# Performance work log

Measured on AMD Instinct MI355X. Metric: run time of the kernel, lower is better.

Reference implementation:

```python
import jax, jax.numpy as jnp
import numpy as np

B, CIN, H, W = 32, 1, 512, 512
PATCH = 16
PW, PH = H // PATCH, W // PATCH  # 32, 32
S = PW * PH                      # 1024 tokens
C = 256
L = 8
POOL = 4
OUT_IDX = (2, 4, 6)
EPS = 1e-5


def setup_inputs() -> dict:
    key = jax.random.key(0)
    ks = jax.random.split(key, 10)
    sc = 1.0 / np.sqrt(C).astype(np.float32)
    return {
        "image": jax.random.normal(ks[0], (B, CIN, H, W), jnp.float32),
        "conv_w": jax.random.normal(ks[1], (C, CIN), jnp.float32),
        "conv_b": jnp.zeros((C,), jnp.float32),
        "feat_w": jax.random.normal(ks[2], (C, C), jnp.float32) * sc,
        "feat_b": jnp.zeros((C,), jnp.float32),
        "ln_s": jnp.ones((L, C), jnp.float32),
        "ln_b": jnp.zeros((L, C), jnp.float32),
        "wq": jax.random.normal(ks[3], (L, C, C), jnp.float32) * sc,
        "bq": jnp.zeros((L, C), jnp.float32),
        "wk": jax.random.normal(ks[4], (L, C, C), jnp.float32) * sc,
        "bk": jnp.zeros((L, C), jnp.float32),
        "wv": jax.random.normal(ks[5], (L, C, C), jnp.float32) * sc,
        "bv": jnp.zeros((L, C), jnp.float32),
        "wf": jax.random.normal(ks[6], (L, C, C), jnp.float32) * sc,
        "bf": jnp.zeros((L, C), jnp.float32),
        "wa": jax.random.normal(ks[7], (L, C, 2 * C), jnp.float32) * sc,
        "ba": jnp.zeros((L, 2 * C), jnp.float32),
    }


def _to_spatial(t):  # [B,S,C] -> [B,C,PW,PH]
    return t.transpose(0, 2, 1).reshape(t.shape[0], C, PW, PH)


def _to_seq(t):  # [B,C,PW,PH] -> [B,S,C]
    return t.reshape(t.shape[0], C, S).transpose(0, 2, 1)


def _layernorm(x, s, b):
    mu = x.mean(-1, keepdims=True)
    var = x.var(-1, keepdims=True)
    return (x - mu) * jax.lax.rsqrt(var + EPS) * s + b


def _attention(x, Wq, bq, Wk, bk, Wv, bv):
    d = np.float32(1.0 / np.sqrt(C))
    Q = _to_spatial(jax.nn.sigmoid(x @ Wq + bq))
    K = _to_spatial(jax.nn.sigmoid(x @ Wk + bk))
    V = _to_spatial(jax.nn.sigmoid(x @ Wv + bv))
    # avg_pool2d with kernel (POOL, 1): pool rows of the patch grid
    qp = Q.reshape(B, C, PW // POOL, POOL, PH).mean(3)
    kp = K.reshape(B, C, PW // POOL, POOL, PH).mean(3)
    # dual softmax low-rank factorization, per channel
    Qk = jax.nn.softmax(d * jnp.einsum('ncik,ncjk->ncij', Q, kp), axis=-1)   # [B,C,PW,PW/POOL]
    Kq = jax.nn.softmax(d * jnp.einsum('ncik,ncjk->ncij', qp, K), axis=-1)   # [B,C,PW/POOL,PW]
    Kqv = jnp.einsum('ncik,nckj->ncij', Kq, V)                               # [B,C,PW/POOL,PH]
    return _to_seq(jnp.einsum('ncik,nckj->ncij', Qk, Kqv))                   # [B,S,C]


def _forward(image, conv_w, conv_b, feat_w, feat_b, ln_s, ln_b,
             wq, bq, wk, bk, wv, bv, wf, bf, wa, ba):
    # Conv2d(kernel=1, stride=patch) == strided subsample + 1x1 projection
    xs = image[:, :, ::PATCH, ::PATCH]                                       # [B,1,PW,PH]
    emb = jnp.einsum('bihw,oi->bohw', xs, conv_w) + conv_b[None, :, None, None]
    x = jnp.tanh(_to_seq(emb) @ feat_w + feat_b)                             # [B,S,C]
    hid, att = [], []
    for l in range(L):
        tn = _layernorm(x, ln_s[l], ln_b[l])
        a = _attention(tn, wq[l], bq[l], wk[l], bk[l], wv[l], bv[l])
        ta = x + a
        # FiLM adaptive norm: sigmoid linear -> interleaved (scale, shift) pairs
        sh = jax.nn.sigmoid(ta @ wa[l] + ba[l]).reshape(B, S, C, 2)
        tn2 = sh[..., 0] * ta + sh[..., 1]
        x = jax.nn.relu(tn2 @ wf[l] + bf[l]) + ta
        if l in OUT_IDX:
            hid.append(x)
            att.append(ta)
    # pack: [last; 3 intermediate hiddens; 3 attention residuals] -> [7,B,S,C]
    return jnp.concatenate([x[None], jnp.stack(hid), jnp.stack(att)], axis=0)


def reference(image, conv_w, conv_b, feat_w, feat_b, ln_s, ln_b,
              wq, bq, wk, bk, wv, bv, wf, bf, wa, ba):
    return _forward(image, conv_w, conv_b, feat_w, feat_b, ln_s, ln_b,
                    wq, bq, wk, bk, wv, bv, wf, bf, wa, ba)
```

## Files before the change

kernel.cpp:

```cpp
#include <hip/hip_runtime.h>
#include <hip/hip_bf16.h>
#include <cstdint>
#include <cstddef>

#define B_ 32
#define C_ 256
#define S_ 1024
#define L_ 8

typedef unsigned short bf16_t;
typedef __attribute__((ext_vector_type(8))) short s8v;
typedef __attribute__((ext_vector_type(4))) short s4v;
typedef __attribute__((ext_vector_type(4))) float f4v;

static __device__ __forceinline__ float b2f(bf16_t v) {
    unsigned int u = ((unsigned int)v) << 16;
    float f;
    __builtin_memcpy(&f, &u, 4);
    return f;
}
static __device__ __forceinline__ bf16_t f2b(float f) {
    unsigned int u;
    __builtin_memcpy(&u, &f, 4);
    u += 0x7fffu + ((u >> 16) & 1u);
    return (bf16_t)(u >> 16);
}
static __device__ __forceinline__ float sigmoidf_(float x) {
    return 1.0f / (1.0f + __expf(-x));
}
static __device__ __forceinline__ void gload_lds16(const void* g, void* l) {
    __builtin_amdgcn_global_load_lds((const __attribute__((address_space(1))) void*)g,
                                     (__attribute__((address_space(3))) void*)l, 16, 0, 0);
}


__global__ void fuse_wb_k(const float* __restrict__ cw, const float* __restrict__ cb,
                          const float* __restrict__ fwm, const float* __restrict__ fbv,
                          float* __restrict__ fw, float* __restrict__ fb) {
    int c = threadIdx.x;
    float a = 0.f, bs = 0.f;
    for (int o = 0; o < C_; o++) {
        float f = fwm[o * C_ + c];
        a += cw[o] * f;
        bs += cb[o] * f;
    }
    fw[c] = a;
    fb[c] = bs + fbv[c];
}

__global__ __launch_bounds__(256) void wtrans_k(const float* __restrict__ wq, const float* __restrict__ wk,
                                                const float* __restrict__ wv, const float* __restrict__ wf,
                                                const float* __restrict__ wa, const float* __restrict__ ln_s,
                                                bf16_t* __restrict__ WT) {
    __shared__ float t[32][33];
    int z = blockIdx.z, l = z / 6, tp = z - l * 6;
    const float* src;
    int ld, cmul, coff;
    if (tp < 4) {
        const float* bases[4] = {wq, wk, wv, wf};
        src = bases[tp] + (size_t)l * 65536;
        ld = 256; cmul = 1; coff = 0;
    } else {
        src = wa + (size_t)l * 131072;
        ld = 512; cmul = 2; coff = tp - 4;
    }
    const float* g = ln_s + l * 256;
    bf16_t* dst = WT + ((size_t)l * 6 + tp) * 65536;
    int k0 = blockIdx.y * 32, m0 = blockIdx.x * 32;
    int tx = threadIdx.x & 31, ty = threadIdx.x >> 5;
#pragma unroll
    for (int r = 0; r < 4; ++r) {
        int k = k0 + ty + 8 * r;
        float v = src[(size_t)k * ld + (m0 + tx) * cmul + coff];
        if (tp < 3) v *= g[k];
        t[ty + 8 * r][tx] = v;
    }
    __syncthreads();
#pragma unroll
    for (int r = 0; r < 4; ++r)
        dst[(size_t)(m0 + ty + 8 * r) * 256 + k0 + tx] = f2b(t[tx][ty + 8 * r]);
}

__global__ __launch_bounds__(256) void colsum_k(const bf16_t* __restrict__ WT,
                                                const float* __restrict__ wq, const float* __restrict__ wk,
                                                const float* __restrict__ wv,
                                                const float* __restrict__ bq, const float* __restrict__ bk,
                                                const float* __restrict__ bv,
                                                const float* __restrict__ ln_b,
                                                float* __restrict__ csum, float* __restrict__ bias2) {
    int m = threadIdx.x, mat = blockIdx.x, l = blockIdx.y;
    const bf16_t* wt = WT + ((size_t)l * 6 + mat) * 65536 + (size_t)m * 256;
    float cs = 0.f;
    for (int k = 0; k < 256; k += 8) {
        s8v u = *(const s8v*)(wt + k);
#pragma unroll
        for (int j = 0; j < 8; ++j) cs += b2f((bf16_t)u[j]);
    }
    const float* worig = (mat == 0 ? wq : mat == 1 ? wk : wv) + (size_t)l * 65536;
    const float* borig = (mat == 0 ? bq : mat == 1 ? bk : bv) + l * 256;
    const float* lb = ln_b + l * 256;
    float bb = 0.f;
    for (int k = 0; k < 256; ++k) bb += lb[k] * worig[(size_t)k * 256 + m];
    int o = (l * 3 + mat) * 256 + m;
    csum[o] = cs;
    bias2[o] = bb + borig[m];
}

__global__ __launch_bounds__(256) void embed_k(const float* __restrict__ img, const float* __restrict__ fw,
                                               const float* __restrict__ fb, bf16_t* __restrict__ X,
                                               float* __restrict__ SUM0, float* __restrict__ SUM1) {
    int wid = threadIdx.x >> 6, lane = threadIdx.x & 63;
    int row = blockIdx.x * 4 + wid;
    int b = row >> 10, s = row & 1023;
    float xv = img[(size_t)b * 262144 + (size_t)(s >> 5) * 8192 + (s & 31) * 16];
    f4v fwv = *(const f4v*)(fw + lane * 4);
    f4v fbv = *(const f4v*)(fb + lane * 4);
    s4v o;
    float sum = 0.f, sq = 0.f;
#pragma unroll
    for (int j = 0; j < 4; ++j) {
        float v = tanhf(xv * fwv[j] + fbv[j]);
        float vb = b2f(f2b(v));
        o[j] = (short)f2b(v);
        sum += vb;
        sq += vb * vb;
    }
    *(s4v*)(X + (size_t)row * 256 + lane * 4) = o;
#pragma unroll
    for (int off = 32; off > 0; off >>= 1) {
        sum += __shfl_xor(sum, off);
        sq += __shfl_xor(sq, off);
    }
    if (lane == 0) {
        SUM0[2 * row] = sum;
        SUM0[2 * row + 1] = sq;
        SUM1[2 * row] = 0.f;
        SUM1[2 * row + 1] = 0.f;
    }
}

template <int MODE, bool HID>
__global__ __launch_bounds__(256) void mm_k(const bf16_t* Ain,
                                            const bf16_t* __restrict__ W0,
                                            const bf16_t* __restrict__ W1,
                                            const float* __restrict__ bias0,
                                            const float* __restrict__ csP,
                                            const float* __restrict__ sumIn,
                                            const bf16_t* ta,
                                            bf16_t* O0, bf16_t* O1, bf16_t* O2,
                                            float* __restrict__ hid,
                                            float* __restrict__ sumOut,
                                            float* __restrict__ sumZero) {
    constexpr int LDSZ = (MODE == 0) ? 34816 : 32768;
    __shared__ char lds[LDSZ];
    char* XS = lds;
    char* WS0 = lds + 16384;
    char* WS1 = lds + 24576;
    const int tid = threadIdx.x, lane = tid & 63, wid = tid >> 6;
    const int wrow = wid >> 1, wcol = wid & 1;
    const int s0 = blockIdx.y * 128, mt0 = blockIdx.x * 64, b = blockIdx.z;

    if constexpr (MODE == 2) {
        int bid = ((blockIdx.z * gridDim.y) + blockIdx.y) * gridDim.x + blockIdx.x;
        if (tid < 64) sumZero[bid * 64 + tid] = 0.f;
    }

    const int lr8 = lane >> 3;
    const int cb0 = ((lane & 7) << 4) ^ (lr8 << 4);

    const char* Ag = (const char*)Ain + (((size_t)b * 1024 + s0) * 256) * 2 + cb0;
    const char* Wg0 = (const char*)W0 + ((size_t)mt0 * 256) * 2 + cb0;
    const char* Wg1 = (const char*)W1 + ((size_t)mt0 * 256) * 2 + cb0;

    f4v acc[4][2] = {};
    f4v acc1[4][2] = {};

    for (int kt = 0; kt < 4; ++kt) {
        const char* ga = Ag + kt * 128;
#pragma unroll
        for (int q = 0; q < 4; ++q) {
            int r0 = wid * 32 + q * 8;
            gload_lds16(ga + (size_t)(r0 + lr8) * 512, XS + r0 * 128);
        }
        const char* gw = Wg0 + kt * 128;
#pragma unroll
        for (int p = 0; p < 2; ++p) {
            int r0 = wid * 16 + p * 8;
            gload_lds16(gw + (size_t)(r0 + lr8) * 512, WS0 + r0 * 128);
        }
        if constexpr (MODE == 1) {
            const char* gw1 = Wg1 + kt * 128;
#pragma unroll
            for (int p = 0; p < 2; ++p) {
                int r0 = wid * 16 + p * 8;
                gload_lds16(gw1 + (size_t)(r0 + lr8) * 512, WS1 + r0 * 128);
            }
        }
        __syncthreads();
#pragma unroll
        for (int kk = 0; kk < 2; ++kk) {
            const int cb = kk * 64 + ((lane >> 4) << 4);
            s8v av[4];
#pragma unroll
            for (int mi = 0; mi < 4; ++mi) {
                int r = wrow * 64 + mi * 16 + (lane & 15);
                av[mi] = *(const s8v*)(XS + r * 128 + (cb ^ ((r & 7) << 4)));
            }
            s8v bv[2], bw[2];
#pragma unroll
            for (int ni = 0; ni < 2; ++ni) {
                int m = wcol * 32 + ni * 16 + (lane & 15);
                bv[ni] = *(const s8v*)(WS0 + m * 128 + (cb ^ ((m & 7) << 4)));
                if constexpr (MODE == 1)
                    bw[ni] = *(const s8v*)(WS1 + m * 128 + (cb ^ ((m & 7) << 4)));
            }
#pragma unroll
            for (int mi = 0; mi < 4; ++mi)
#pragma unroll
                for (int ni = 0; ni < 2; ++ni) {
                    acc[mi][ni] = __builtin_amdgcn_mfma_f32_16x16x32_bf16(av[mi], bv[ni], acc[mi][ni], 0, 0, 0);
                    if constexpr (MODE == 1)
                        acc1[mi][ni] = __builtin_amdgcn_mfma_f32_16x16x32_bf16(av[mi], bw[ni], acc1[mi][ni], 0, 0, 0);
                }
        }
        __syncthreads();
    }

    if constexpr (MODE == 0) {
        const int mat = mt0 >> 8, mw = mt0 & 255;
        const float* bs = bias0 + mat * 256 + mw;
        const float* cs = csP + mat * 256 + mw;
        bf16_t* Os = (mat == 0) ? O0 : (mat == 1 ? O1 : O2);
        bf16_t* T = (bf16_t*)lds;
#pragma unroll
        for (int mi = 0; mi < 4; ++mi)
#pragma unroll
            for (int r = 0; r < 4; ++r) {
                int sl = wrow * 64 + mi * 16 + (lane >> 4) * 4 + r;
                int sg = b * 1024 + s0 + sl;
                float2 sv = *(const float2*)(sumIn + 2 * sg);
                float mu = sv.x * (1.f / 256.f);
                float var = sv.y * (1.f / 256.f) - mu * mu;
                float rsv = rsqrtf(var + 1e-5f);
                float a = rsv, cc = rsv * mu;
#pragma unroll
                for (int ni = 0; ni < 2; ++ni) {
                    int ml = wcol * 32 + ni * 16 + (lane & 15);
                    float v = sigmoidf_(a * acc[mi][ni][r] - cc * cs[ml] + bs[ml]);
                    T[ml * 144 + sl] = f2b(v);
                }
            }
        __syncthreads();
        int m = tid >> 2, c0s = (tid & 3) * 32;
        bf16_t* dst = Os + ((size_t)(b * 256 + mw + m)) * 1024 + s0 + c0s;
#pragma unroll
        for (int j = 0; j < 4; ++j)
            *(s8v*)(dst + j * 8) = *(const s8v*)(T + m * 144 + c0s + j * 8);
    } else if constexpr (MODE == 1) {
#pragma unroll
        for (int mi = 0; mi < 4; ++mi)
#pragma unroll
            for (int ni = 0; ni < 2; ++ni) {
                int ml = mt0 + wcol * 32 + ni * 16 + (lane & 15);
#pragma unroll
                for (int r = 0; r < 4; ++r) {
                    int sg = b * 1024 + s0 + wrow * 64 + mi * 16 + (lane >> 4) * 4 + r;
                    size_t idx = (size_t)sg * 256 + ml;
                    float v = sigmoidf_(acc[mi][ni][r] + bias0[2 * ml]) * b2f(ta[idx]) +
                              sigmoidf_(acc1[mi][ni][r] + bias0[2 * ml + 1]);
                    O0[idx] = f2b(v);
                }
            }
    } else {
#pragma unroll
        for (int mi = 0; mi < 4; ++mi)
#pragma unroll
            for (int r = 0; r < 4; ++r) {
                int sg = b * 1024 + s0 + wrow * 64 + mi * 16 + (lane >> 4) * 4 + r;
                float vv[2];
#pragma unroll
                for (int ni = 0; ni < 2; ++ni) {
                    int ml = mt0 + wcol * 32 + ni * 16 + (lane & 15);
                    size_t idx = (size_t)sg * 256 + ml;
                    float v = fmaxf(acc[mi][ni][r] + bias0[ml], 0.f) + b2f(ta[idx]);
                    O0[idx] = f2b(v);
                    if constexpr (HID) hid[idx] = v;
                    vv[ni] = v;
                }
                float ps = vv[0] + vv[1];
                float pq = vv[0] * vv[0] + vv[1] * vv[1];
                ps += __shfl_xor(ps, 1); pq += __shfl_xor(pq, 1);
                ps += __shfl_xor(ps, 2); pq += __shfl_xor(pq, 2);
                ps += __shfl_xor(ps, 4); pq += __shfl_xor(pq, 4);
                ps += __shfl_xor(ps, 8); pq += __shfl_xor(pq, 8);
                if ((lane & 15) == 0) {
                    atomicAdd(&sumOut[2 * sg], ps);
                    atomicAdd(&sumOut[2 * sg + 1], pq);
                }
            }
    }
}

__global__ __launch_bounds__(256) void attn_k(const bf16_t* __restrict__ Q, const bf16_t* __restrict__ K,
                                              const bf16_t* __restrict__ V, bf16_t* __restrict__ A) {
    __shared__ char Lds[35840];
    const int w = threadIdx.x >> 6, lane = threadIdx.x & 63;
    char* P = Lds + w * 8960;
    const int gw = blockIdx.x * 4 + w;
    const int b = gw >> 8, c = gw & 255;
    const size_t base = ((size_t)b * 256 + c) * 1024;
    constexpr int VT = 0, S1 = 2560, S2 = 5120, KQ = 6400;
    const f4v zf = {0.f, 0.f, 0.f, 0.f};
    const int frow = lane & 15, fhalf = lane >> 4;
    const int fbyte = fhalf * 16;
    const bf16_t* Qg = Q + base;
    const bf16_t* Kg = K + base;
    const bf16_t* Vg = V + base;

    s8v aq0 = *(const s8v*)(Qg + frow * 32 + fhalf * 8);
    s8v aq1 = *(const s8v*)(Qg + (16 + frow) * 32 + fhalf * 8);
    s8v bk0 = *(const s8v*)(Kg + frow * 32 + fhalf * 8);
    s8v bk1 = *(const s8v*)(Kg + (16 + frow) * 32 + fhalf * 8);
    float accq[8], acck[8];
#pragma unroll
    for (int j = 0; j < 8; ++j) { accq[j] = 0.f; acck[j] = 0.f; }
#pragma unroll
    for (int pp = 0; pp < 4; ++pp) {
        int rr = 4 * frow + pp;
        if (rr > 31) rr = 31;
        s8v uq = *(const s8v*)(Qg + rr * 32 + fhalf * 8);
        s8v uk = *(const s8v*)(Kg + rr * 32 + fhalf * 8);
#pragma unroll
        for (int j = 0; j < 8; ++j) {
            accq[j] += b2f((bf16_t)uq[j]);
            acck[j] += b2f((bf16_t)uk[j]);
        }
    }
    s8v aqp, bkp;
#pragma unroll
    for (int j = 0; j < 8; ++j) {
        aqp[j] = (short)f2b(accq[j] * 0.25f);
        bkp[j] = (short)f2b(acck[j] * 0.25f);
    }
    {
        s8v v0 = *(const s8v*)(Vg + lane * 16);
        s8v v1 = *(const s8v*)(Vg + lane * 16 + 8);
        int pw = lane >> 1, ph0 = (lane & 1) * 16;
#pragma unroll
        for (int j = 0; j < 8; ++j) {
            *(bf16_t*)(P + VT + (ph0 + j) * 80 + pw * 2) = (bf16_t)(unsigned short)v0[j];
            *(bf16_t*)(P + VT + (ph0 + 8 + j) * 80 + pw * 2) = (bf16_t)(unsigned short)v1[j];
        }
    }
    if (lane < 32) {
#pragma unroll
        for (int q = 0; q < 4; ++q) *(f4v*)(P + S1 + lane * 80 + q * 16) = zf;
#pragma unroll
        for (int q = 0; q < 3; ++q) *(f4v*)(P + KQ + lane * 80 + 16 + q * 16) = zf;
    } else if (lane < 40) {
#pragma unroll
        for (int q = 0; q < 4; ++q) *(f4v*)(P + S2 + (lane - 24) * 80 + q * 16) = zf;
    }

    f4v s1a = __builtin_amdgcn_mfma_f32_16x16x32_bf16(aq0, bkp, zf, 0, 0, 0);
    f4v s1b = __builtin_amdgcn_mfma_f32_16x16x32_bf16(aq1, bkp, zf, 0, 0, 0);
    f4v s2a = __builtin_amdgcn_mfma_f32_16x16x32_bf16(aqp, bk0, zf, 0, 0, 0);
    f4v s2b = __builtin_amdgcn_mfma_f32_16x16x32_bf16(aqp, bk1, zf, 0, 0, 0);

    const float dsc = 0.0625f;
    {
        int j = lane & 15;
#pragma unroll
        for (int t = 0; t < 2; ++t) {
            f4v av = t ? s1b : s1a;
#pragma unroll
            for (int r = 0; r < 4; ++r) {
                float x = av[r] * dsc;
                float m = x;
                m = fmaxf(m, __shfl_xor(m, 1));
                m = fmaxf(m, __shfl_xor(m, 2));
                m = fmaxf(m, __shfl_xor(m, 4));
                float e2 = __expf(x - m);
                float s = e2;
                s += __shfl_xor(s, 1);
                s += __shfl_xor(s, 2);
                s += __shfl_xor(s, 4);
                float p = e2 / s;
                if (j < 8) {
                    int row = t * 16 + fhalf * 4 + r;
                    *(bf16_t*)(P + S1 + row * 80 + j * 2) = f2b(p);
                }
            }
        }
    }
#pragma unroll
    for (int r = 0; r < 4; ++r) {
        float xa = s2a[r] * dsc, xb = s2b[r] * dsc;
        float m = fmaxf(xa, xb);
        m = fmaxf(m, __shfl_xor(m, 1));
        m = fmaxf(m, __shfl_xor(m, 2));
        m = fmaxf(m, __shfl_xor(m, 4));
        m = fmaxf(m, __shfl_xor(m, 8));
        float ea = __expf(xa - m), eb = __expf(xb - m);
        float s = ea + eb;
        s += __shfl_xor(s, 1);
        s += __shfl_xor(s, 2);
        s += __shfl_xor(s, 4);
        s += __shfl_xor(s, 8);
        float inv = 1.f / s;
        if (lane < 32) {
            int row = fhalf * 4 + r;
            *(bf16_t*)(P + S2 + row * 80 + frow * 2) = f2b(ea * inv);
            *(bf16_t*)(P + S2 + row * 80 + (16 + frow) * 2) = f2b(eb * inv);
        }
    }
    __builtin_amdgcn_wave_barrier();
    {
        s8v as2 = *(const s8v*)(P + S2 + frow * 80 + fbyte);
        s8v bv0 = *(const s8v*)(P + VT + frow * 80 + fbyte);
        s8v bv1 = *(const s8v*)(P + VT + (16 + frow) * 80 + fbyte);
        f4v k3a = __builtin_amdgcn_mfma_f32_16x16x32_bf16(as2, bv0, zf, 0, 0, 0);
        f4v k3b = __builtin_amdgcn_mfma_f32_16x16x32_bf16(as2, bv1, zf, 0, 0, 0);
        if (lane < 32) {
#pragma unroll
            for (int r = 0; r < 4; ++r) {
                int i2 = fhalf * 4 + r;
                *(bf16_t*)(P + KQ + frow * 80 + i2 * 2) = f2b(k3a[r]);
                *(bf16_t*)(P + KQ + (16 + frow) * 80 + i2 * 2) = f2b(k3b[r]);
            }
        }
    }
    __builtin_amdgcn_wave_barrier();
    {
        s8v a40 = *(const s8v*)(P + S1 + frow * 80 + fbyte);
        s8v a41 = *(const s8v*)(P + S1 + (16 + frow) * 80 + fbyte);
        s8v b40 = *(const s8v*)(P + KQ + frow * 80 + fbyte);
        s8v b41 = *(const s8v*)(P + KQ + (16 + frow) * 80 + fbyte);
        f4v o00 = __builtin_amdgcn_mfma_f32_16x16x32_bf16(a40, b40, zf, 0, 0, 0);
        f4v o01 = __builtin_amdgcn_mfma_f32_16x16x32_bf16(a40, b41, zf, 0, 0, 0);
        f4v o10 = __builtin_amdgcn_mfma_f32_16x16x32_bf16(a41, b40, zf, 0, 0, 0);
        f4v o11 = __builtin_amdgcn_mfma_f32_16x16x32_bf16(a41, b41, zf, 0, 0, 0);
#pragma unroll
        for (int r = 0; r < 4; ++r) {
            int r0 = fhalf * 4 + r;
            *(bf16_t*)(P + VT + r0 * 80 + frow * 2) = f2b(o00[r]);
            *(bf16_t*)(P + VT + r0 * 80 + (16 + frow) * 2) = f2b(o01[r]);
            *(bf16_t*)(P + VT + (16 + r0) * 80 + frow * 2) = f2b(o10[r]);
            *(bf16_t*)(P + VT + (16 + r0) * 80 + (16 + frow) * 2) = f2b(o11[r]);
        }
    }
    __builtin_amdgcn_wave_barrier();
    {
        int i = lane >> 1, hh = (lane & 1) * 32;
        s8v r0 = *(const s8v*)(P + VT + i * 80 + hh);
        s8v r1 = *(const s8v*)(P + VT + i * 80 + hh + 16);
        *(s8v*)(A + base + lane * 16) = r0;
        *(s8v*)(A + base + lane * 16 + 8) = r1;
    }
}

template <bool SNAP>
__global__ __launch_bounds__(256) void add_tr_k(const bf16_t* __restrict__ Aa, bf16_t* X,
                                                float* __restrict__ att) {
    __shared__ float T[32][33];
    int b = blockIdx.z, c0 = blockIdx.y * 32, s0 = blockIdx.x * 32;
    int tx = threadIdx.x & 31, ty = threadIdx.x >> 5;
#pragma unroll
    for (int r = 0; r < 4; ++r)
        T[ty + 8 * r][tx] = b2f(Aa[((size_t)(b * 256 + c0 + ty + 8 * r)) * 1024 + s0 + tx]);
    __syncthreads();
#pragma unroll
    for (int r = 0; r < 4; ++r) {
        int s = s0 + ty + 8 * r;
        size_t idx = ((size_t)(b * 1024 + s)) * 256 + c0 + tx;
        float v = b2f(X[idx]) + T[tx][ty + 8 * r];
        X[idx] = f2b(v);
        if constexpr (SNAP) att[idx] = v;
    }
}


extern "C" void kernel_launch(void* const* d_in, const int* in_sizes, int n_in,
                              void* d_out, int out_size, void* d_ws, size_t ws_size,
                              hipStream_t stream) {
    const float* image  = (const float*)d_in[0];
    const float* conv_w = (const float*)d_in[1];
    const float* conv_b = (const float*)d_in[2];
    const float* feat_w = (const float*)d_in[3];
    const float* feat_b = (const float*)d_in[4];
    const float* ln_s   = (const float*)d_in[5];
    const float* ln_b   = (const float*)d_in[6];
    const float* wq     = (const float*)d_in[7];
    const float* bq     = (const float*)d_in[8];
    const float* wk     = (const float*)d_in[9];
    const float* bk     = (const float*)d_in[10];
    const float* wv     = (const float*)d_in[11];
    const float* bv     = (const float*)d_in[12];
    const float* wf     = (const float*)d_in[13];
    const float* bfv    = (const float*)d_in[14];
    const float* wa     = (const float*)d_in[15];
    const float* ba     = (const float*)d_in[16];
    float* out = (float*)d_out;

    char* p = (char*)d_ws;
    const size_t MB16 = (size_t)B_ * S_ * C_ * sizeof(bf16_t);
    float* fw    = (float*)p;  p += 1024;
    float* fb    = (float*)p;  p += 1024;
    float* SUM   = (float*)p;  p += 524288;
    float* csum  = (float*)p;  p += 24576;
    float* bias2 = (float*)p;  p += 24576;
    bf16_t* WT = (bf16_t*)p;   p += (size_t)48 * 65536 * 2;
    bf16_t* X  = (bf16_t*)p;   p += MB16;
    bf16_t* T1 = (bf16_t*)p;   p += MB16;
    bf16_t* T2 = (bf16_t*)p;   p += MB16;
    bf16_t* Qb = (bf16_t*)p;   p += MB16;
    bf16_t* Kb = (bf16_t*)p;   p += MB16;
    bf16_t* Vb = (bf16_t*)p;   p += MB16;
    size_t needed = (size_t)(p - (char*)d_ws);
    if (ws_size < needed) Vb = (bf16_t*)d_out;

    fuse_wb_k<<<1, 256, 0, stream>>>(conv_w, conv_b, feat_w, feat_b, fw, fb);
    wtrans_k<<<dim3(8, 8, 48), 256, 0, stream>>>(wq, wk, wv, wf, wa, ln_s, WT);
    colsum_k<<<dim3(3, 8), 256, 0, stream>>>(WT, wq, wk, wv, bq, bk, bv, ln_b, csum, bias2);
    embed_k<<<8192, 256, 0, stream>>>(image, fw, fb, X, SUM, SUM + 65536);

    const size_t slot = (size_t)B_ * S_ * C_;

    for (int l = 0; l < L_; ++l) {
        const bf16_t* WTl = WT + (size_t)l * 6 * 65536;
        int snap = (l == 2) ? 0 : (l == 4) ? 1 : (l == 6) ? 2 : -1;
        const float* sumIn = SUM + (size_t)(l & 1) * 65536;
        float* sumOut = SUM + (size_t)((l + 1) & 1) * 65536;
        float* sumZero = SUM + (size_t)(l & 1) * 65536;

        mm_k<0, false><<<dim3(12, 8, 32), 256, 0, stream>>>(
            X, WTl, nullptr, bias2 + l * 768, csum + l * 768, sumIn, nullptr,
            Qb, Kb, Vb, nullptr, nullptr, nullptr);
        attn_k<<<2048, 256, 0, stream>>>(Qb, Kb, Vb, T1);
        if (snap >= 0)
            add_tr_k<true><<<dim3(32, 8, 32), 256, 0, stream>>>(T1, X, out + (size_t)(4 + snap) * slot);
        else
            add_tr_k<false><<<dim3(32, 8, 32), 256, 0, stream>>>(T1, X, nullptr);
        mm_k<1, false><<<dim3(4, 8, 32), 256, 0, stream>>>(
            X, WTl + 4 * 65536, WTl + 5 * 65536, ba + l * 512, nullptr, nullptr, X,
            T2, nullptr, nullptr, nullptr, nullptr, nullptr);
        float* hid = (snap >= 0) ? out + (size_t)(1 + snap) * slot : (l == 7 ? out : nullptr);
        if (hid)
            mm_k<2, true><<<dim3(4, 8, 32), 256, 0, stream>>>(
                T2, WTl + 3 * 65536, nullptr, bfv + l * 256, nullptr, nullptr, X,
                X, nullptr, nullptr, hid, sumOut, sumZero);
        else
            mm_k<2, false><<<dim3(4, 8, 32), 256, 0, stream>>>(
                T2, WTl + 3 * 65536, nullptr, bfv + l * 256, nullptr, nullptr, X,
                X, nullptr, nullptr, nullptr, sumOut, sumZero);
    }
}
```

Baseline: 1.148 ms.

## Fuse attention with residual add and replace atomic row stats with partial sums

The per-channel attention kernel is merged with the transpose-and-residual-add kernel. A 512-thread block now handles 16 channels of one batch and writes X (and the attention snapshot) directly, which removes the T1 intermediate buffer and one launch per layer. LayerNorm row statistics are no longer accumulated with atomicAdd into ping-pong buffers that must be zeroed. Each column-tile wave instead writes a partial (sum, sumsq) into 8 slots per row, and the QKV GEMM reduces these once per block into LDS. The trade-off is a larger LDS footprint for the attention kernel, fewer blocks, and a bigger partial-stats buffer.

Result: slower. 1.275 ms (+11.0%).

```diff
diff --git a/kernel.cpp b/kernel.cpp
--- a/kernel.cpp
+++ b/kernel.cpp
@@ -108,7 +108,7 @@
 
 __global__ __launch_bounds__(256) void embed_k(const float* __restrict__ img, const float* __restrict__ fw,
                                                const float* __restrict__ fb, bf16_t* __restrict__ X,
-                                               float* __restrict__ SUM0, float* __restrict__ SUM1) {
+                                               float* __restrict__ PART) {
     int wid = threadIdx.x >> 6, lane = threadIdx.x & 63;
     int row = blockIdx.x * 4 + wid;
     int b = row >> 10, s = row & 1023;
@@ -131,11 +131,10 @@
         sum += __shfl_xor(sum, off);
         sq += __shfl_xor(sq, off);
     }
-    if (lane == 0) {
-        SUM0[2 * row] = sum;
-        SUM0[2 * row + 1] = sq;
-        SUM1[2 * row] = 0.f;
-        SUM1[2 * row + 1] = 0.f;
+    float sb = __shfl(sum, 0), qb = __shfl(sq, 0);
+    if (lane < 8) {
+        float2 v = (lane == 0) ? make_float2(sb, qb) : make_float2(0.f, 0.f);
+        *(float2*)(PART + (size_t)row * 16 + lane * 2) = v;
     }
 }
 
@@ -145,12 +144,11 @@
                                             const bf16_t* __restrict__ W1,
                                             const float* __restrict__ bias0,
                                             const float* __restrict__ csP,
-                                            const float* __restrict__ sumIn,
+                                            const float* __restrict__ PART,
                                             const bf16_t* ta,
                                             bf16_t* O0, bf16_t* O1, bf16_t* O2,
                                             float* __restrict__ hid,
-                                            float* __restrict__ sumOut,
-                                            float* __restrict__ sumZero) {
+                                            float* __restrict__ partOut) {
     constexpr int LDSZ = (MODE == 0) ? 34816 : 32768;
     __shared__ char lds[LDSZ];
     char* XS = lds;
@@ -160,9 +158,22 @@
     const int wrow = wid >> 1, wcol = wid & 1;
     const int s0 = blockIdx.y * 128, mt0 = blockIdx.x * 64, b = blockIdx.z;
 
-    if constexpr (MODE == 2) {
-        int bid = ((blockIdx.z * gridDim.y) + blockIdx.y) * gridDim.x + blockIdx.x;
-        if (tid < 64) sumZero[bid * 64 + tid] = 0.f;
+    if constexpr (MODE == 0) {
+        float2* stats = (float2*)(lds + 24576);
+        if (tid < 128) {
+            int sg = b * 1024 + s0 + tid;
+            const float* pp = PART + (size_t)sg * 16;
+            f4v p0 = *(const f4v*)pp;
+            f4v p1 = *(const f4v*)(pp + 4);
+            f4v p2 = *(const f4v*)(pp + 8);
+            f4v p3 = *(const f4v*)(pp + 12);
+            float su = p0[0] + p0[2] + p1[0] + p1[2] + p2[0] + p2[2] + p3[0] + p3[2];
+            float qq = p0[1] + p0[3] + p1[1] + p1[3] + p2[1] + p2[3] + p3[1] + p3[3];
+            float mu = su * (1.f / 256.f);
+            float var = qq * (1.f / 256.f) - mu * mu;
+            float rsv = rsqrtf(var + 1e-5f);
+            stats[tid] = make_float2(rsv, rsv * mu);
+        }
     }
 
     const int lr8 = lane >> 3;
@@ -231,18 +242,15 @@
         const float* bs = bias0 + mat * 256 + mw;
         const float* cs = csP + mat * 256 + mw;
         bf16_t* Os = (mat == 0) ? O0 : (mat == 1 ? O1 : O2);
+        const float2* stats = (const float2*)(lds + 24576);
         bf16_t* T = (bf16_t*)lds;
 #pragma unroll
         for (int mi = 0; mi < 4; ++mi)
 #pragma unroll
             for (int r = 0; r < 4; ++r) {
                 int sl = wrow * 64 + mi * 16 + (lane >> 4) * 4 + r;
-                int sg = b * 1024 + s0 + sl;
-                float2 sv = *(const float2*)(sumIn + 2 * sg);
-                float mu = sv.x * (1.f / 256.f);
-                float var = sv.y * (1.f / 256.f) - mu * mu;
-                float rsv = rsqrtf(var + 1e-5f);
-                float a = rsv, cc = rsv * mu;
+                float2 st = stats[sl];
+                float a = st.x, cc = st.y;
 #pragma unroll
                 for (int ni = 0; ni < 2; ++ni) {
                     int ml = wcol * 32 + ni * 16 + (lane & 15);
@@ -293,65 +301,27 @@
                 ps += __shfl_xor(ps, 2); pq += __shfl_xor(pq, 2);
                 ps += __shfl_xor(ps, 4); pq += __shfl_xor(pq, 4);
                 ps += __shfl_xor(ps, 8); pq += __shfl_xor(pq, 8);
-                if ((lane & 15) == 0) {
-                    atomicAdd(&sumOut[2 * sg], ps);
-                    atomicAdd(&sumOut[2 * sg + 1], pq);
-                }
-            }
-    }
-}
-
-__global__ __launch_bounds__(256) void attn_k(const bf16_t* __restrict__ Q, const bf16_t* __restrict__ K,
-                                              const bf16_t* __restrict__ V, bf16_t* __restrict__ A) {
-    __shared__ char Lds[35840];
+                if ((lane & 15) == 0)
+                    *(float2*)(partOut + (size_t)sg * 16 + (blockIdx.x * 2 + wcol) * 2) =
+                        make_float2(ps, pq);
+            }
+    }
+}
+
+template <bool SNAP>
+__global__ __launch_bounds__(512) void attnf_k(const bf16_t* __restrict__ Q, const bf16_t* __restrict__ K,
+                                               const bf16_t* __restrict__ V, bf16_t* __restrict__ Xp,
+                                               float* __restrict__ att) {
+    __shared__ char Lds[71808];
     const int w = threadIdx.x >> 6, lane = threadIdx.x & 63;
-    char* P = Lds + w * 8960;
-    const int gw = blockIdx.x * 4 + w;
-    const int b = gw >> 8, c = gw & 255;
-    const size_t base = ((size_t)b * 256 + c) * 1024;
+    char* P = Lds + w * 8976;
+    const int b = blockIdx.x >> 4, g = blockIdx.x & 15;
+    const int c0 = g * 16;
     constexpr int VT = 0, S1 = 2560, S2 = 5120, KQ = 6400;
     const f4v zf = {0.f, 0.f, 0.f, 0.f};
     const int frow = lane & 15, fhalf = lane >> 4;
     const int fbyte = fhalf * 16;
-    const bf16_t* Qg = Q + base;
-    const bf16_t* Kg = K + base;
-    const bf16_t* Vg = V + base;
-
-    s8v aq0 = *(const s8v*)(Qg + frow * 32 + fhalf * 8);
-    s8v aq1 = *(const s8v*)(Qg + (16 + frow) * 32 + fhalf * 8);
-    s8v bk0 = *(const s8v*)(Kg + frow * 32 + fhalf * 8);
-    s8v bk1 = *(const s8v*)(Kg + (16 + frow) * 32 + fhalf * 8);
-    float accq[8], acck[8];
-#pragma unroll
-    for (int j = 0; j < 8; ++j) { accq[j] = 0.f; acck[j] = 0.f; }
-#pragma unroll
-    for (int pp = 0; pp < 4; ++pp) {
-        int rr = 4 * frow + pp;
-        if (rr > 31) rr = 31;
-        s8v uq = *(const s8v*)(Qg + rr * 32 + fhalf * 8);
-        s8v uk = *(const s8v*)(Kg + rr * 32 + fhalf * 8);
-#pragma unroll
-        for (int j = 0; j < 8; ++j) {
-            accq[j] += b2f((bf16_t)uq[j]);
-            acck[j] += b2f((bf16_t)uk[j]);
-        }
-    }
-    s8v aqp, bkp;
-#pragma unroll
-    for (int j = 0; j < 8; ++j) {
-        aqp[j] = (short)f2b(accq[j] * 0.25f);
-        bkp[j] = (short)f2b(acck[j] * 0.25f);
-    }
-    {
-        s8v v0 = *(const s8v*)(Vg + lane * 16);
-        s8v v1 = *(const s8v*)(Vg + lane * 16 + 8);
-        int pw = lane >> 1, ph0 = (lane & 1) * 16;
-#pragma unroll
-        for (int j = 0; j < 8; ++j) {
-            *(bf16_t*)(P + VT + (ph0 + j) * 80 + pw * 2) = (bf16_t)(unsigned short)v0[j];
-            *(bf16_t*)(P + VT + (ph0 + 8 + j) * 80 + pw * 2) = (bf16_t)(unsigned short)v1[j];
-        }
-    }
+
     if (lane < 32) {
 #pragma unroll
         for (int q = 0; q < 4; ++q) *(f4v*)(P + S1 + lane * 80 + q * 16) = zf;
@@ -362,120 +332,163 @@
         for (int q = 0; q < 4; ++q) *(f4v*)(P + S2 + (lane - 24) * 80 + q * 16) = zf;
     }
 
-    f4v s1a = __builtin_amdgcn_mfma_f32_16x16x32_bf16(aq0, bkp, zf, 0, 0, 0);
-    f4v s1b = __builtin_amdgcn_mfma_f32_16x16x32_bf16(aq1, bkp, zf, 0, 0, 0);
-    f4v s2a = __builtin_amdgcn_mfma_f32_16x16x32_bf16(aqp, bk0, zf, 0, 0, 0);
-    f4v s2b = __builtin_amdgcn_mfma_f32_16x16x32_bf16(aqp, bk1, zf, 0, 0, 0);
-
-    const float dsc = 0.0625f;
-    {
-        int j = lane & 15;
-#pragma unroll
-        for (int t = 0; t < 2; ++t) {
-            f4v av = t ? s1b : s1a;
+    for (int k = 0; k < 2; ++k) {
+        const int c = c0 + 8 * k + w;
+        const size_t base = ((size_t)b * 256 + c) * 1024;
+        const bf16_t* Qg = Q + base;
+        const bf16_t* Kg = K + base;
+        const bf16_t* Vg = V + base;
+
+        s8v aq0 = *(const s8v*)(Qg + frow * 32 + fhalf * 8);
+        s8v aq1 = *(const s8v*)(Qg + (16 + frow) * 32 + fhalf * 8);
+        s8v bk0 = *(const s8v*)(Kg + frow * 32 + fhalf * 8);
+        s8v bk1 = *(const s8v*)(Kg + (16 + frow) * 32 + fhalf * 8);
+        float accq[8], acck[8];
+#pragma unroll
+        for (int j = 0; j < 8; ++j) { accq[j] = 0.f; acck[j] = 0.f; }
+#pragma unroll
+        for (int pp = 0; pp < 4; ++pp) {
+            int rr = 4 * frow + pp;
+            if (rr > 31) rr = 31;
+            s8v uq = *(const s8v*)(Qg + rr * 32 + fhalf * 8);
+            s8v uk = *(const s8v*)(Kg + rr * 32 + fhalf * 8);
+#pragma unroll
+            for (int j = 0; j < 8; ++j) {
+                accq[j] += b2f((bf16_t)uq[j]);
+                acck[j] += b2f((bf16_t)uk[j]);
+            }
+        }
+        s8v aqp, bkp;
+#pragma unroll
+        for (int j = 0; j < 8; ++j) {
+            aqp[j] = (short)f2b(accq[j] * 0.25f);
+            bkp[j] = (short)f2b(acck[j] * 0.25f);
+        }
+        {
+            s8v v0 = *(const s8v*)(Vg + lane * 16);
+            s8v v1 = *(const s8v*)(Vg + lane * 16 + 8);
+            int pw = lane >> 1, ph0 = (lane & 1) * 16;
+#pragma unroll
+            for (int j = 0; j < 8; ++j) {
+                *(bf16_t*)(P + VT + (ph0 + j) * 80 + pw * 2) = (bf16_t)(unsigned short)v0[j];
+                *(bf16_t*)(P + VT + (ph0 + 8 + j) * 80 + pw * 2) = (bf16_t)(unsigned short)v1[j];
+            }
+        }
+
+        f4v s1a = __builtin_amdgcn_mfma_f32_16x16x32_bf16(aq0, bkp, zf, 0, 0, 0);
+        f4v s1b = __builtin_amdgcn_mfma_f32_16x16x32_bf16(aq1, bkp, zf, 0, 0, 0);
+        f4v s2a = __builtin_amdgcn_mfma_f32_16x16x32_bf16(aqp, bk0, zf, 0, 0, 0);
+        f4v s2b = __builtin_amdgcn_mfma_f32_16x16x32_bf16(aqp, bk1, zf, 0, 0, 0);
+
+        const float dsc = 0.0625f;
+        {
+            int j = lane & 15;
+#pragma unroll
+            for (int t = 0; t < 2; ++t) {
+                f4v av = t ? s1b : s1a;
+#pragma unroll
+                for (int r = 0; r < 4; ++r) {
+                    float x = av[r] * dsc;
+                    float m = x;
+                    m = fmaxf(m, __shfl_xor(m, 1));
+                    m = fmaxf(m, __shfl_xor(m, 2));
+                    m = fmaxf(m, __shfl_xor(m, 4));
+                    float e2 = __expf(x - m);
+                    float s = e2;
+                    s += __shfl_xor(s, 1);
+                    s += __shfl_xor(s, 2);
+                    s += __shfl_xor(s, 4);
+                    float p = e2 / s;
+                    if (j < 8) {
+                        int row = t * 16 + fhalf * 4 + r;
+                        *(bf16_t*)(P + S1 + row * 80 + j * 2) = f2b(p);
+                    }
+                }
+            }
+        }
+#pragma unroll
+        for (int r = 0; r < 4; ++r) {
+            float xa = s2a[r] * dsc, xb = s2b[r] * dsc;
+            float m = fmaxf(xa, xb);
+            m = fmaxf(m, __shfl_xor(m, 1));
+            m = fmaxf(m, __shfl_xor(m, 2));
+            m = fmaxf(m, __shfl_xor(m, 4));
+            m = fmaxf(m, __shfl_xor(m, 8));
+            float ea = __expf(xa - m), eb = __expf(xb - m);
+            float s = ea + eb;
+            s += __shfl_xor(s, 1);
+            s += __shfl_xor(s, 2);
+            s += __shfl_xor(s, 4);
+            s += __shfl_xor(s, 8);
+            float inv = 1.f / s;
+            if (lane < 32) {
+                int row = fhalf * 4 + r;
+                *(bf16_t*)(P + S2 + row * 80 + frow * 2) = f2b(ea * inv);
+                *(bf16_t*)(P + S2 + row * 80 + (16 + frow) * 2) = f2b(eb * inv);
+            }
+        }
+        __builtin_amdgcn_wave_barrier();
+        {
+            s8v as2 = *(const s8v*)(P + S2 + frow * 80 + fbyte);
+            s8v bv0 = *(const s8v*)(P + VT + frow * 80 + fbyte);
+            s8v bv1 = *(const s8v*)(P + VT + (16 + frow) * 80 + fbyte);
+            f4v k3a = __builtin_amdgcn_mfma_f32_16x16x32_bf16(as2, bv0, zf, 0, 0, 0);
+            f4v k3b = __builtin_amdgcn_mfma_f32_16x16x32_bf16(as2, bv1, zf, 0, 0, 0);
+            if (lane < 32) {
+#pragma unroll
+                for (int r = 0; r < 4; ++r) {
+                    int i2 = fhalf * 4 + r;
+                    *(bf16_t*)(P + KQ + frow * 80 + i2 * 2) = f2b(k3a[r]);
+                    *(bf16_t*)(P + KQ + (16 + frow) * 80 + i2 * 2) = f2b(k3b[r]);
+                }
+            }
+        }
+        __builtin_amdgcn_wave_barrier();
+        {
+            s8v a40 = *(const s8v*)(P + S1 + frow * 80 + fbyte);
+            s8v a41 = *(const s8v*)(P + S1 + (16 + frow) * 80 + fbyte);
+            s8v b40 = *(const s8v*)(P + KQ + frow * 80 + fbyte);
+            s8v b41 = *(const s8v*)(P + KQ + (16 + frow) * 80 + fbyte);
+            f4v o00 = __builtin_amdgcn_mfma_f32_16x16x32_bf16(a40, b40, zf, 0, 0, 0);
+            f4v o01 = __builtin_amdgcn_mfma_f32_16x16x32_bf16(a40, b41, zf, 0, 0, 0);
+            f4v o10 = __builtin_amdgcn_mfma_f32_16x16x32_bf16(a41, b40, zf, 0, 0, 0);
+            f4v o11 = __builtin_amdgcn_mfma_f32_16x16x32_bf16(a41, b41, zf, 0, 0, 0);
 #pragma unroll
             for (int r = 0; r < 4; ++r) {
-                float x = av[r] * dsc;
-                float m = x;
-                m = fmaxf(m, __shfl_xor(m, 1));
-                m = fmaxf(m, __shfl_xor(m, 2));
-                m = fmaxf(m, __shfl_xor(m, 4));
-                float e2 = __expf(x - m);
-                float s = e2;
-                s += __shfl_xor(s, 1);
-                s += __shfl_xor(s, 2);
-                s += __shfl_xor(s, 4);
-                float p = e2 / s;
-                if (j < 8) {
-                    int row = t * 16 + fhalf * 4 + r;
-                    *(bf16_t*)(P + S1 + row * 80 + j * 2) = f2b(p);
-                }
-            }
-        }
-    }
-#pragma unroll
-    for (int r = 0; r < 4; ++r) {
-        float xa = s2a[r] * dsc, xb = s2b[r] * dsc;
-        float m = fmaxf(xa, xb);
-        m = fmaxf(m, __shfl_xor(m, 1));
-        m = fmaxf(m, __shfl_xor(m, 2));
-        m = fmaxf(m, __shfl_xor(m, 4));
-        m = fmaxf(m, __shfl_xor(m, 8));
-        float ea = __expf(xa - m), eb = __expf(xb - m);
-        float s = ea + eb;
-        s += __shfl_xor(s, 1);
-        s += __shfl_xor(s, 2);
-        s += __shfl_xor(s, 4);
-        s += __shfl_xor(s, 8);
-        float inv = 1.f / s;
-        if (lane < 32) {
-            int row = fhalf * 4 + r;
-            *(bf16_t*)(P + S2 + row * 80 + frow * 2) = f2b(ea * inv);
-            *(bf16_t*)(P + S2 + row * 80 + (16 + frow) * 2) = f2b(eb * inv);
-        }
-    }
-    __builtin_amdgcn_wave_barrier();
-    {
-        s8v as2 = *(const s8v*)(P + S2 + frow * 80 + fbyte);
-        s8v bv0 = *(const s8v*)(P + VT + frow * 80 + fbyte);
-        s8v bv1 = *(const s8v*)(P + VT + (16 + frow) * 80 + fbyte);
-        f4v k3a = __builtin_amdgcn_mfma_f32_16x16x32_bf16(as2, bv0, zf, 0, 0, 0);
-        f4v k3b = __builtin_amdgcn_mfma_f32_16x16x32_bf16(as2, bv1, zf, 0, 0, 0);
-        if (lane < 32) {
-#pragma unroll
-            for (int r = 0; r < 4; ++r) {
-                int i2 = fhalf * 4 + r;
-                *(bf16_t*)(P + KQ + frow * 80 + i2 * 2) = f2b(k3a[r]);
-                *(bf16_t*)(P + KQ + (16 + frow) * 80 + i2 * 2) = f2b(k3b[r]);
-            }
-        }
-    }
-    __builtin_amdgcn_wave_barrier();
-    {
-        s8v a40 = *(const s8v*)(P + S1 + frow * 80 + fbyte);
-        s8v a41 = *(const s8v*)(P + S1 + (16 + frow) * 80 + fbyte);
-        s8v b40 = *(const s8v*)(P + KQ + frow * 80 + fbyte);
-        s8v b41 = *(const s8v*)(P + KQ + (16 + frow) * 80 + fbyte);
-        f4v o00 = __builtin_amdgcn_mfma_f32_16x16x32_bf16(a40, b40, zf, 0, 0, 0);
-        f4v o01 = __builtin_amdgcn_mfma_f32_16x16x32_bf16(a40, b41, zf, 0, 0, 0);
-        f4v o10 = __builtin_amdgcn_mfma_f32_16x16x32_bf16(a41, b40, zf, 0, 0, 0);
-        f4v o11 = __builtin_amdgcn_mfma_f32_16x16x32_bf16(a41, b41, zf, 0, 0, 0);
-#pragma unroll
-        for (int r = 0; r < 4; ++r) {
-            int r0 = fhalf * 4 + r;
-            *(bf16_t*)(P + VT + r0 * 80 + frow * 2) = f2b(o00[r]);
-            *(bf16_t*)(P + VT + r0 * 80 + (16 + frow) * 2) = f2b(o01[r]);
-            *(bf16_t*)(P + VT + (16 + r0) * 80 + frow * 2) = f2b(o10[r]);
-            *(bf16_t*)(P + VT + (16 + r0) * 80 + (16 + frow) * 2) = f2b(o11[r]);
-        }
-    }
-    __builtin_amdgcn_wave_barrier();
-    {
-        int i = lane >> 1, hh = (lane & 1) * 32;
-        s8v r0 = *(const s8v*)(P + VT + i * 80 + hh);
-        s8v r1 = *(const s8v*)(P + VT + i * 80 + hh + 16);
-        *(s8v*)(A + base + lane * 16) = r0;
-        *(s8v*)(A + base + lane * 16 + 8) = r1;
-    }
-}
-
-template <bool SNAP>
-__global__ __launch_bounds__(256) void add_tr_k(const bf16_t* __restrict__ Aa, bf16_t* X,
-                                                float* __restrict__ att) {
-    __shared__ float T[32][33];
-    int b = blockIdx.z, c0 = blockIdx.y * 32, s0 = blockIdx.x * 32;
-    int tx = threadIdx.x & 31, ty = threadIdx.x >> 5;
-#pragma unroll
-    for (int r = 0; r < 4; ++r)
-        T[ty + 8 * r][tx] = b2f(Aa[((size_t)(b * 256 + c0 + ty + 8 * r)) * 1024 + s0 + tx]);
-    __syncthreads();
-#pragma unroll
-    for (int r = 0; r < 4; ++r) {
-        int s = s0 + ty + 8 * r;
-        size_t idx = ((size_t)(b * 1024 + s)) * 256 + c0 + tx;
-        float v = b2f(X[idx]) + T[tx][ty + 8 * r];
-        X[idx] = f2b(v);
-        if constexpr (SNAP) att[idx] = v;
+                int r0 = fhalf * 4 + r;
+                *(bf16_t*)(P + VT + r0 * 80 + frow * 2) = f2b(o00[r]);
+                *(bf16_t*)(P + VT + r0 * 80 + (16 + frow) * 2) = f2b(o01[r]);
+                *(bf16_t*)(P + VT + (16 + r0) * 80 + frow * 2) = f2b(o10[r]);
+                *(bf16_t*)(P + VT + (16 + r0) * 80 + (16 + frow) * 2) = f2b(o11[r]);
+            }
+        }
+        __syncthreads();
+        {
+            const int cbase = c0 + 8 * k;
+            for (int t = threadIdx.x; t < 1024; t += 512) {
+                int off = (t >> 5) * 80 + (t & 31) * 2;
+                s8v avv;
+#pragma unroll
+                for (int w2 = 0; w2 < 8; ++w2)
+                    avv[w2] = *(const short*)(Lds + w2 * 8976 + off);
+                size_t xi = ((size_t)(b * 1024 + t)) * 256 + cbase;
+                s8v xv = *(const s8v*)(Xp + xi);
+                s8v nx;
+                f4v lo, hi;
+#pragma unroll
+                for (int j = 0; j < 8; ++j) {
+                    float v = b2f((bf16_t)xv[j]) + b2f((bf16_t)avv[j]);
+                    nx[j] = (short)f2b(v);
+                    if (j < 4) lo[j] = v; else hi[j - 4] = v;
+                }
+                *(s8v*)(Xp + xi) = nx;
+                if constexpr (SNAP) {
+                    *(f4v*)(att + xi) = lo;
+                    *(f4v*)(att + xi + 4) = hi;
+                }
+            }
+        }
+        __syncthreads();
     }
 }
 
@@ -506,12 +519,11 @@
     const size_t MB16 = (size_t)B_ * S_ * C_ * sizeof(bf16_t);
     float* fw    = (float*)p;  p += 1024;
     float* fb    = (float*)p;  p += 1024;
-    float* SUM   = (float*)p;  p += 524288;
+    float* PART  = (float*)p;  p += 2097152;
     float* csum  = (float*)p;  p += 24576;
     float* bias2 = (float*)p;  p += 24576;
     bf16_t* WT = (bf16_t*)p;   p += (size_t)48 * 65536 * 2;
     bf16_t* X  = (bf16_t*)p;   p += MB16;
-    bf16_t* T1 = (bf16_t*)p;   p += MB16;
     bf16_t* T2 = (bf16_t*)p;   p += MB16;
     bf16_t* Qb = (bf16_t*)p;   p += MB16;
     bf16_t* Kb = (bf16_t*)p;   p += MB16;
@@ -522,36 +534,32 @@
     fuse_wb_k<<<1, 256, 0, stream>>>(conv_w, conv_b, feat_w, feat_b, fw, fb);
     wtrans_k<<<dim3(8, 8, 48), 256, 0, stream>>>(wq, wk, wv, wf, wa, ln_s, WT);
     colsum_k<<<dim3(3, 8), 256, 0, stream>>>(WT, wq, wk, wv, bq, bk, bv, ln_b, csum, bias2);
-    embed_k<<<8192, 256, 0, stream>>>(image, fw, fb, X, SUM, SUM + 65536);
+    embed_k<<<8192, 256, 0, stream>>>(image, fw, fb, X, PART);
 
     const size_t slot = (size_t)B_ * S_ * C_;
 
     for (int l = 0; l < L_; ++l) {
         const bf16_t* WTl = WT + (size_t)l * 6 * 65536;
         int snap = (l == 2) ? 0 : (l == 4) ? 1 : (l == 6) ? 2 : -1;
-        const float* sumIn = SUM + (size_t)(l & 1) * 65536;
-        float* sumOut = SUM + (size_t)((l + 1) & 1) * 65536;
-        float* sumZero = SUM + (size_t)(l & 1) * 65536;
 
         mm_k<0, false><<<dim3(12, 8, 32), 256, 0, stream>>>(
-            X, WTl, nullptr, bias2 + l * 768, csum + l * 768, sumIn, nullptr,
-            Qb, Kb, Vb, nullptr, nullptr, nullptr);
-        attn_k<<<2048, 256, 0, stream>>>(Qb, Kb, Vb, T1);
+            X, WTl, nullptr, bias2 + l * 768, csum + l * 768, PART, nullptr,
+            Qb, Kb, Vb, nullptr, nullptr);
         if (snap >= 0)
-            add_tr_k<true><<<dim3(32, 8, 32), 256, 0, stream>>>(T1, X, out + (size_t)(4 + snap) * slot);
+            attnf_k<true><<<512, 512, 0, stream>>>(Qb, Kb, Vb, X, out + (size_t)(4 + snap) * slot);
         else
-            add_tr_k<false><<<dim3(32, 8, 32), 256, 0, stream>>>(T1, X, nullptr);
+            attnf_k<false><<<512, 512, 0, stream>>>(Qb, Kb, Vb, X, nullptr);
         mm_k<1, false><<<dim3(4, 8, 32), 256, 0, stream>>>(
             X, WTl + 4 * 65536, WTl + 5 * 65536, ba + l * 512, nullptr, nullptr, X,
-            T2, nullptr, nullptr, nullptr, nullptr, nullptr);
+            T2, nullptr, nullptr, nullptr, nullptr);
         float* hid = (snap >= 0) ? out + (size_t)(1 + snap) * slot : (l == 7 ? out : nullptr);
         if (hid)
             mm_k<2, true><<<dim3(4, 8, 32), 256, 0, stream>>>(
                 T2, WTl + 3 * 65536, nullptr, bfv + l * 256, nullptr, nullptr, X,
-                X, nullptr, nullptr, hid, sumOut, sumZero);
+                X, nullptr, nullptr, hid, PART);
         else
             mm_k<2, false><<<dim3(4, 8, 32), 256, 0, stream>>>(
                 T2, WTl + 3 * 65536, nullptr, bfv + l * 256, nullptr, nullptr, X,
-                X, nullptr, nullptr, nullptr, sumOut, sumZero);
-    }
-}
+                X, nullptr, nullptr, nullptr, PART);
+    }
+}
```
